# Performance work log

Hardware: AMD Instinct MI355X
Metric: run time of the kernel (lower is better)

The kernel has to match this reference:

```python
import jax, jax.numpy as jnp
import numpy as np

B, C_IN, C_OUT, E, K = 4, 32, 64, 200000, 5


def setup_inputs() -> dict:
    key = jax.random.key(0)
    k1, k2, k3, k4 = jax.random.split(key, 4)
    x = jax.random.normal(k1, (B, C_IN, E), dtype=jnp.float32)
    # Gi: per-edge [self_id, n1, n2, n3, n4] one-ring indices into the edge axis
    Gi = jax.random.randint(k2, (B, E, K), 0, E, dtype=jnp.int32)
    # Conv2d(C_IN, C_OUT, kernel_size=(1, K)) weights, PyTorch layout (O, I, 1, K)
    fan_in = C_IN * K
    bound = 1.0 / np.sqrt(fan_in)
    W = jax.random.uniform(k3, (C_OUT, C_IN, 1, K), jnp.float32, -bound, bound)
    b = jax.random.uniform(k4, (C_OUT,), jnp.float32, -bound, bound)
    return {"x": x, "Gi": Gi, "W": W, "b": b}


def _mesh_conv(x, Gi, W, b):
    Bn, C, En = x.shape
    # prepend zero-padding column (index 0 after Gi+1 maps to zeros)
    xp = jnp.concatenate([jnp.zeros((Bn, C, 1), x.dtype), x], axis=2)  # (B, C, E+1)
    idx = Gi.astype(jnp.int32) + 1  # (B, E, 5)
    # gather 1-ring neighbor features: f[b, c, e, j] = xp[b, c, idx[b, e, j]]
    f = jax.vmap(lambda xb, ib: xb[:, ib])(xp, idx)  # (B, C, E, 5)
    f0, f1, f2, f3, f4 = (f[..., j] for j in range(5))
    # symmetric, order-invariant combine
    G = jnp.stack([f0, f1 + f3, f2 + f4, jnp.abs(f1 - f3), jnp.abs(f2 - f4)], axis=3)
    # Conv2d with kernel (1, K), no padding -> contraction over (C_in, K)
    out = jnp.einsum('bcek,ock->boe', G, W[:, :, 0, :]) + b[None, :, None]
    return out[..., None]  # (B, C_out, E, 1)


def reference(x, Gi, W, b):
    return _mesh_conv(x, Gi, W, b)
```

## Files before the change

### kernel.cpp

```cpp
#include <hip/hip_runtime.h>

typedef unsigned int u32;
typedef __bf16 bf16x8 __attribute__((ext_vector_type(8)));
typedef float f32x4 __attribute__((ext_vector_type(4)));
typedef u32 u32x4 __attribute__((ext_vector_type(4)));

#define B_DIM 4
#define E_DIM 200000
#define C_OUT 64
#define TPB   12500
#define NTILE (B_DIM * TPB)
#define KPADW 168
#define ROWU  (KPADW / 2)
#define WLDS  (C_OUT * ROWU)

__device__ __forceinline__ u32 pack_bf2(float lo, float hi) {
  u32 a = __float_as_uint(lo) + 0x8000u;
  u32 b = __float_as_uint(hi) + 0x8000u;
  return __builtin_amdgcn_perm(b, a, 0x07060302u);
}

__device__ __forceinline__ u32 absdiff_pack(u32 a, u32 b) {
  float alo = __uint_as_float(a << 16), ahi = __uint_as_float(a & 0xffff0000u);
  float blo = __uint_as_float(b << 16), bhi = __uint_as_float(b & 0xffff0000u);
  u32 dlo = __float_as_uint(alo - blo) + 0x8000u;
  u32 dhi = __float_as_uint(ahi - bhi) + 0x8000u;
  return __builtin_amdgcn_perm(dhi, dlo, 0x07060302u) & 0x7fff7fffu;
}

__global__ __launch_bounds__(256) void xpose_kernel(const float* __restrict__ x,
                                                    u32* __restrict__ xT) {
  const int e = blockIdx.x * 256 + threadIdx.x;
  const int b = blockIdx.y;
  if (e >= E_DIM) return;
  const float* xb = x + (size_t)b * 32 * E_DIM;
  u32 row[16];
#pragma unroll
  for (int u = 0; u < 16; ++u) {
    const float lo = xb[(2 * u) * E_DIM + e];
    const float hi = xb[(2 * u + 1) * E_DIM + e];
    row[u] = pack_bf2(lo, hi);
  }
  uint4* dst = (uint4*)(xT + ((size_t)b * E_DIM + e) * 16);
#pragma unroll
  for (int w = 0; w < 4; ++w)
    dst[w] = make_uint4(row[4 * w], row[4 * w + 1], row[4 * w + 2], row[4 * w + 3]);
}

__global__ __launch_bounds__(256) void prep_w(const float* __restrict__ W,
                                              u32* __restrict__ Wa) {
  const int p = blockIdx.x * 256 + threadIdx.x;
  if (p >= C_OUT * 5 * 16) return;
  const int o = p / 80, r = p % 80, s = r / 16, cc = r % 16;
  const float w0 = W[(o * 32 + 2 * cc) * 5 + s];
  const float w1 = W[(o * 32 + 2 * cc + 1) * 5 + s];
  Wa[o * ROWU + s * 16 + cc] = pack_bf2(w0, w1);
}

__global__ __launch_bounds__(256, 4) void mesh_main(const u32* __restrict__ xT,
                                                    const int* __restrict__ Gi,
                                                    const u32* __restrict__ Wa,
                                                    const float* __restrict__ bias,
                                                    float* __restrict__ out) {
  __shared__ u32 Wl[WLDS];
  for (int i = threadIdx.x; i < WLDS; i += 256) Wl[i] = Wa[i];
  __syncthreads();

  const int l  = threadIdx.x & 63;
  const int wv = threadIdx.x >> 6;
  const int n  = l & 15;
  const int q  = l >> 4;
  const int j4 = l & 3;
  const int eL = l >> 2;
  const int pidx = ((n << 2) | q) << 2;
  const int NW = gridDim.x * 4;

  int t = blockIdx.x * 4 + wv;

  int b  = t / TPB;
  int e0 = (t - b * TPB) * 16;
  {
  }
  const int* gp = Gi + ((b * E_DIM + e0 + eL) * 5);
  int i0 = gp[0], i1 = gp[1], i2 = gp[2], i3 = gp[3], i4 = gp[4];
  const uint4* xb = (const uint4*)(xT + (size_t)b * E_DIM * 16);
  uint4 c0 = xb[i0 * 4 + j4], c1 = xb[i1 * 4 + j4], c2 = xb[i2 * 4 + j4],
        c3 = xb[i3 * 4 + j4], c4 = xb[i4 * 4 + j4];

  const f32x4* bp = (const f32x4*)bias;

  for (;;) {
    const int nt = t + NW;
    const bool has = nt < NTILE;
    int nb = 0, ne0 = 0;
    uint4 x0, x1, x2, x3, x4;
    if (has) {
      nb  = nt / TPB;
      ne0 = (nt - nb * TPB) * 16;
      const int* gq = Gi + ((nb * E_DIM + ne0 + eL) * 5);
      const int k0 = gq[0], k1 = gq[1], k2 = gq[2], k3 = gq[3], k4 = gq[4];
      const uint4* xn = (const uint4*)(xT + (size_t)nb * E_DIM * 16);
      x0 = xn[k0 * 4 + j4]; x1 = xn[k1 * 4 + j4]; x2 = xn[k2 * 4 + j4];
      x3 = xn[k3 * 4 + j4]; x4 = xn[k4 * 4 + j4];
    }

    u32 rows[7][4];
    rows[0][0] = c0.x; rows[0][1] = c0.y; rows[0][2] = c0.z; rows[0][3] = c0.w;
    rows[1][0] = c1.x; rows[1][1] = c1.y; rows[1][2] = c1.z; rows[1][3] = c1.w;
    rows[2][0] = c2.x; rows[2][1] = c2.y; rows[2][2] = c2.z; rows[2][3] = c2.w;
    rows[3][0] = c3.x; rows[3][1] = c3.y; rows[3][2] = c3.z; rows[3][3] = c3.w;
    rows[4][0] = c4.x; rows[4][1] = c4.y; rows[4][2] = c4.z; rows[4][3] = c4.w;
#pragma unroll
    for (int wd = 0; wd < 4; ++wd) {
      rows[5][wd] = absdiff_pack(rows[1][wd], rows[3][wd]);
      rows[6][wd] = absdiff_pack(rows[2][wd], rows[4][wd]);
    }

    f32x4 acc0 = bp[0 * 4 + q];
    f32x4 acc1 = bp[1 * 4 + q];
    f32x4 acc2 = bp[2 * 4 + q];
    f32x4 acc3 = bp[3 * 4 + q];

    const int aslot[7] = {0, 1, 2, 1, 2, 3, 4};
#pragma unroll
    for (int kc = 0; kc < 7; ++kc) {
      union { u32 u[4]; bf16x8 v; } bu;
#pragma unroll
      for (int c = 0; c < 4; ++c)
        bu.u[c] = (u32)__builtin_amdgcn_ds_bpermute(pidx, (int)rows[kc][c]);
      const int wbase = n * ROWU + aslot[kc] * 16 + q * 4;
      union { u32x4 u; bf16x8 v; } a0, a1, a2, a3;
      a0.u = *(const u32x4*)(Wl + wbase);
      a1.u = *(const u32x4*)(Wl + wbase + 16 * ROWU);
      a2.u = *(const u32x4*)(Wl + wbase + 32 * ROWU);
      a3.u = *(const u32x4*)(Wl + wbase + 48 * ROWU);
      acc0 = __builtin_amdgcn_mfma_f32_16x16x32_bf16(a0.v, bu.v, acc0, 0, 0, 0);
      acc1 = __builtin_amdgcn_mfma_f32_16x16x32_bf16(a1.v, bu.v, acc1, 0, 0, 0);
      acc2 = __builtin_amdgcn_mfma_f32_16x16x32_bf16(a2.v, bu.v, acc2, 0, 0, 0);
      acc3 = __builtin_amdgcn_mfma_f32_16x16x32_bf16(a3.v, bu.v, acc3, 0, 0, 0);
    }

    float* ob = out + ((b * C_OUT + q * 4) * E_DIM + e0 + n);
#pragma unroll
    for (int r = 0; r < 4; ++r) {
      ob[(0 * 16 + r) * E_DIM] = acc0[r];
      ob[(1 * 16 + r) * E_DIM] = acc1[r];
      ob[(2 * 16 + r) * E_DIM] = acc2[r];
      ob[(3 * 16 + r) * E_DIM] = acc3[r];
    }

    if (!has) break;
    t = nt; b = nb; e0 = ne0;
    c0 = x0; c1 = x1; c2 = x2; c3 = x3; c4 = x4;
  }
}

extern "C" void kernel_launch(void* const* d_in, const int* in_sizes, int n_in,
                              void* d_out, int out_size, void* d_ws, size_t ws_size,
                              hipStream_t stream) {
  const float* x    = (const float*)d_in[0];
  const int*   Gi   = (const int*)d_in[1];
  const float* W    = (const float*)d_in[2];
  const float* bias = (const float*)d_in[3];
  float* out = (float*)d_out;

  u32* xT = (u32*)d_ws;
  u32* Wa = xT + (size_t)B_DIM * E_DIM * 16;

  dim3 gx((E_DIM + 255) / 256, B_DIM);
  xpose_kernel<<<gx, 256, 0, stream>>>(x, xT);

  prep_w<<<(C_OUT * 5 * 16 + 255) / 256, 256, 0, stream>>>(W, Wa);

  mesh_main<<<1024, 256, 0, stream>>>(xT, Gi, Wa, bias, out);
}
```

Before: 459.0 us.

## Gather MFMA B-fragments directly, pre-swizzle weights, stage transpose through LDS

Each lane now loads the neighbor feature chunk it needs for the MFMA B operand straight from global memory, which removes the ds_bpermute shuffles. The weights are pre-expanded into 7 k-slices laid out per lane so LDS reads are contiguous uint4s. The transpose kernel now goes through LDS so its global stores are coalesced. The index prefetch runs two tiles ahead, the bias is hoisted into registers, and the grid size and occupancy bound change. The cost is more gather requests per lane pattern, higher register pressure, and a larger LDS weight buffer.

```diff
diff --git a/kernel.cpp b/kernel.cpp
--- a/kernel.cpp
+++ b/kernel.cpp
@@ -3,16 +3,14 @@
 typedef unsigned int u32;
 typedef __bf16 bf16x8 __attribute__((ext_vector_type(8)));
 typedef float f32x4 __attribute__((ext_vector_type(4)));
-typedef u32 u32x4 __attribute__((ext_vector_type(4)));
 
 #define B_DIM 4
 #define E_DIM 200000
 #define C_OUT 64
 #define TPB   12500
-#define NTILE (B_DIM * TPB)
-#define KPADW 168
-#define ROWU  (KPADW / 2)
-#define WLDS  (C_OUT * ROWU)
+#define NT    (B_DIM * TPB)
+#define NBLK  1280
+#define WLDS_U4 1792
 
 __device__ __forceinline__ u32 pack_bf2(float lo, float hi) {
   u32 a = __float_as_uint(lo) + 0x8000u;
@@ -28,130 +26,155 @@
   return __builtin_amdgcn_perm(dhi, dlo, 0x07060302u) & 0x7fff7fffu;
 }
 
+__device__ __forceinline__ uint4 absdiff_vec(uint4 a, uint4 b) {
+  return make_uint4(absdiff_pack(a.x, b.x), absdiff_pack(a.y, b.y),
+                    absdiff_pack(a.z, b.z), absdiff_pack(a.w, b.w));
+}
+
 __global__ __launch_bounds__(256) void xpose_kernel(const float* __restrict__ x,
                                                     u32* __restrict__ xT) {
-  const int e = blockIdx.x * 256 + threadIdx.x;
+  __shared__ u32 T[256 * 17];
   const int b = blockIdx.y;
-  if (e >= E_DIM) return;
-  const float* xb = x + (size_t)b * 32 * E_DIM;
-  u32 row[16];
+  const int e0 = blockIdx.x * 256;
+  const int t = threadIdx.x;
+  const int nrows = min(256, E_DIM - e0);
+  const float* xb = x + (size_t)b * 32 * E_DIM + e0;
+  if (t < nrows) {
 #pragma unroll
-  for (int u = 0; u < 16; ++u) {
-    const float lo = xb[(2 * u) * E_DIM + e];
-    const float hi = xb[(2 * u + 1) * E_DIM + e];
-    row[u] = pack_bf2(lo, hi);
+    for (int u = 0; u < 16; ++u) {
+      const float lo = xb[(size_t)(2 * u) * E_DIM + t];
+      const float hi = xb[(size_t)(2 * u + 1) * E_DIM + t];
+      T[t * 17 + u] = pack_bf2(lo, hi);
+    }
   }
-  uint4* dst = (uint4*)(xT + ((size_t)b * E_DIM + e) * 16);
+  __syncthreads();
+  const int total = nrows * 16;
+  u32* dst = xT + ((size_t)b * E_DIM + e0) * 16;
 #pragma unroll
-  for (int w = 0; w < 4; ++w)
-    dst[w] = make_uint4(row[4 * w], row[4 * w + 1], row[4 * w + 2], row[4 * w + 3]);
+  for (int k = 0; k < 16; ++k) {
+    const int g = t + k * 256;
+    if (g < total) dst[g] = T[(g >> 4) * 17 + (g & 15)];
+  }
 }
 
 __global__ __launch_bounds__(256) void prep_w(const float* __restrict__ W,
-                                              u32* __restrict__ Wa) {
+                                              u32* __restrict__ Wa2) {
   const int p = blockIdx.x * 256 + threadIdx.x;
-  if (p >= C_OUT * 5 * 16) return;
-  const int o = p / 80, r = p % 80, s = r / 16, cc = r % 16;
-  const float w0 = W[(o * 32 + 2 * cc) * 5 + s];
-  const float w1 = W[(o * 32 + 2 * cc + 1) * 5 + s];
-  Wa[o * ROWU + s * 16 + cc] = pack_bf2(w0, w1);
+  if (p >= 7168) return;
+  const int r = p & 3;
+  const int o = (p >> 2) & 63;
+  const int q = (p >> 8) & 3;
+  const int s = p >> 10;
+  const int kmap[7] = {0, 1, 2, 1, 2, 3, 4};
+  const int c0 = q * 8 + 2 * r;
+  const float w0 = W[(o * 32 + c0) * 5 + kmap[s]];
+  const float w1 = W[(o * 32 + c0 + 1) * 5 + kmap[s]];
+  Wa2[p] = pack_bf2(w0, w1);
 }
 
-__global__ __launch_bounds__(256, 4) void mesh_main(const u32* __restrict__ xT,
-                                                    const int* __restrict__ Gi,
-                                                    const u32* __restrict__ Wa,
-                                                    const float* __restrict__ bias,
-                                                    float* __restrict__ out) {
-  __shared__ u32 Wl[WLDS];
-  for (int i = threadIdx.x; i < WLDS; i += 256) Wl[i] = Wa[i];
+__global__ __launch_bounds__(256) void mesh_main(const u32* __restrict__ xT,
+                                                 const int* __restrict__ Gi,
+                                                 const u32* __restrict__ Wa2,
+                                                 const float* __restrict__ bias,
+                                                 float* __restrict__ out) {
+  __shared__ uint4 Wl[WLDS_U4];
+  {
+    const uint4* src = (const uint4*)Wa2;
+#pragma unroll
+    for (int k = 0; k < 7; ++k) Wl[threadIdx.x + k * 256] = src[threadIdx.x + k * 256];
+  }
   __syncthreads();
 
-  const int l  = threadIdx.x & 63;
+  const int l = threadIdx.x & 63;
   const int wv = threadIdx.x >> 6;
-  const int n  = l & 15;
-  const int q  = l >> 4;
-  const int j4 = l & 3;
-  const int eL = l >> 2;
-  const int pidx = ((n << 2) | q) << 2;
-  const int NW = gridDim.x * 4;
+  const int n = l & 15;
+  const int q = l >> 4;
+  const int NW = NBLK * 4;
+
+  f32x4 bv[4];
+#pragma unroll
+  for (int og = 0; og < 4; ++og) bv[og] = *(const f32x4*)(bias + og * 16 + q * 4);
+
+  const uint4* xb4 = (const uint4*)xT;
 
   int t = blockIdx.x * 4 + wv;
 
-  int b  = t / TPB;
-  int e0 = (t - b * TPB) * 16;
+  int gcur[5], gnext[5];
   {
+    const int b = t / TPB;
+    const int e = (t - b * TPB) * 16 + n;
+    const int* gp = Gi + (b * E_DIM + e) * 5;
+#pragma unroll
+    for (int s = 0; s < 5; ++s) gcur[s] = b * E_DIM + gp[s];
   }
-  const int* gp = Gi + ((b * E_DIM + e0 + eL) * 5);
-  int i0 = gp[0], i1 = gp[1], i2 = gp[2], i3 = gp[3], i4 = gp[4];
-  const uint4* xb = (const uint4*)(xT + (size_t)b * E_DIM * 16);
-  uint4 c0 = xb[i0 * 4 + j4], c1 = xb[i1 * 4 + j4], c2 = xb[i2 * 4 + j4],
-        c3 = xb[i3 * 4 + j4], c4 = xb[i4 * 4 + j4];
+  uint4 cur[5];
+#pragma unroll
+  for (int s = 0; s < 5; ++s) cur[s] = xb4[(size_t)gcur[s] * 4 + q];
 
-  const f32x4* bp = (const f32x4*)bias;
+  int t1 = t + NW;
+  if (t1 < NT) {
+    const int b = t1 / TPB;
+    const int e = (t1 - b * TPB) * 16 + n;
+    const int* gp = Gi + (b * E_DIM + e) * 5;
+#pragma unroll
+    for (int s = 0; s < 5; ++s) gnext[s] = b * E_DIM + gp[s];
+  }
 
   for (;;) {
-    const int nt = t + NW;
-    const bool has = nt < NTILE;
-    int nb = 0, ne0 = 0;
-    uint4 x0, x1, x2, x3, x4;
+    const bool has = t1 < NT;
+    uint4 nxt[5];
     if (has) {
-      nb  = nt / TPB;
-      ne0 = (nt - nb * TPB) * 16;
-      const int* gq = Gi + ((nb * E_DIM + ne0 + eL) * 5);
-      const int k0 = gq[0], k1 = gq[1], k2 = gq[2], k3 = gq[3], k4 = gq[4];
-      const uint4* xn = (const uint4*)(xT + (size_t)nb * E_DIM * 16);
-      x0 = xn[k0 * 4 + j4]; x1 = xn[k1 * 4 + j4]; x2 = xn[k2 * 4 + j4];
-      x3 = xn[k3 * 4 + j4]; x4 = xn[k4 * 4 + j4];
+#pragma unroll
+      for (int s = 0; s < 5; ++s) nxt[s] = xb4[(size_t)gnext[s] * 4 + q];
+    }
+    const int t2 = t1 + NW;
+    if (t2 < NT) {
+      const int b = t2 / TPB;
+      const int e = (t2 - b * TPB) * 16 + n;
+      const int* gp = Gi + (b * E_DIM + e) * 5;
+#pragma unroll
+      for (int s = 0; s < 5; ++s) gnext[s] = b * E_DIM + gp[s];
     }
 
-    u32 rows[7][4];
-    rows[0][0] = c0.x; rows[0][1] = c0.y; rows[0][2] = c0.z; rows[0][3] = c0.w;
-    rows[1][0] = c1.x; rows[1][1] = c1.y; rows[1][2] = c1.z; rows[1][3] = c1.w;
-    rows[2][0] = c2.x; rows[2][1] = c2.y; rows[2][2] = c2.z; rows[2][3] = c2.w;
-    rows[3][0] = c3.x; rows[3][1] = c3.y; rows[3][2] = c3.z; rows[3][3] = c3.w;
-    rows[4][0] = c4.x; rows[4][1] = c4.y; rows[4][2] = c4.z; rows[4][3] = c4.w;
+    union { uint4 u; bf16x8 v; } frag[7];
 #pragma unroll
-    for (int wd = 0; wd < 4; ++wd) {
-      rows[5][wd] = absdiff_pack(rows[1][wd], rows[3][wd]);
-      rows[6][wd] = absdiff_pack(rows[2][wd], rows[4][wd]);
+    for (int s = 0; s < 5; ++s) frag[s].u = cur[s];
+    frag[5].u = absdiff_vec(cur[1], cur[3]);
+    frag[6].u = absdiff_vec(cur[2], cur[4]);
+
+    f32x4 acc0 = bv[0], acc1 = bv[1], acc2 = bv[2], acc3 = bv[3];
+#pragma unroll
+    for (int c = 0; c < 7; ++c) {
+      const uint4* wp = Wl + (c * 4 + q) * 64 + n;
+      union { uint4 u; bf16x8 v; } a0, a1, a2, a3;
+      a0.u = wp[0];
+      a1.u = wp[16];
+      a2.u = wp[32];
+      a3.u = wp[48];
+      acc0 = __builtin_amdgcn_mfma_f32_16x16x32_bf16(a0.v, frag[c].v, acc0, 0, 0, 0);
+      acc1 = __builtin_amdgcn_mfma_f32_16x16x32_bf16(a1.v, frag[c].v, acc1, 0, 0, 0);
+      acc2 = __builtin_amdgcn_mfma_f32_16x16x32_bf16(a2.v, frag[c].v, acc2, 0, 0, 0);
+      acc3 = __builtin_amdgcn_mfma_f32_16x16x32_bf16(a3.v, frag[c].v, acc3, 0, 0, 0);
     }
 
-    f32x4 acc0 = bp[0 * 4 + q];
-    f32x4 acc1 = bp[1 * 4 + q];
-    f32x4 acc2 = bp[2 * 4 + q];
-    f32x4 acc3 = bp[3 * 4 + q];
-
-    const int aslot[7] = {0, 1, 2, 1, 2, 3, 4};
+    {
+      const int b = t / TPB;
+      const int e0 = (t - b * TPB) * 16;
+      float* ob = out + ((size_t)(b * C_OUT + q * 4) * E_DIM + e0 + n);
 #pragma unroll
-    for (int kc = 0; kc < 7; ++kc) {
-      union { u32 u[4]; bf16x8 v; } bu;
-#pragma unroll
-      for (int c = 0; c < 4; ++c)
-        bu.u[c] = (u32)__builtin_amdgcn_ds_bpermute(pidx, (int)rows[kc][c]);
-      const int wbase = n * ROWU + aslot[kc] * 16 + q * 4;
-      union { u32x4 u; bf16x8 v; } a0, a1, a2, a3;
-      a0.u = *(const u32x4*)(Wl + wbase);
-      a1.u = *(const u32x4*)(Wl + wbase + 16 * ROWU);
-      a2.u = *(const u32x4*)(Wl + wbase + 32 * ROWU);
-      a3.u = *(const u32x4*)(Wl + wbase + 48 * ROWU);
-      acc0 = __builtin_amdgcn_mfma_f32_16x16x32_bf16(a0.v, bu.v, acc0, 0, 0, 0);
-      acc1 = __builtin_amdgcn_mfma_f32_16x16x32_bf16(a1.v, bu.v, acc1, 0, 0, 0);
-      acc2 = __builtin_amdgcn_mfma_f32_16x16x32_bf16(a2.v, bu.v, acc2, 0, 0, 0);
-      acc3 = __builtin_amdgcn_mfma_f32_16x16x32_bf16(a3.v, bu.v, acc3, 0, 0, 0);
-    }
-
-    float* ob = out + ((b * C_OUT + q * 4) * E_DIM + e0 + n);
-#pragma unroll
-    for (int r = 0; r < 4; ++r) {
-      ob[(0 * 16 + r) * E_DIM] = acc0[r];
-      ob[(1 * 16 + r) * E_DIM] = acc1[r];
-      ob[(2 * 16 + r) * E_DIM] = acc2[r];
-      ob[(3 * 16 + r) * E_DIM] = acc3[r];
+      for (int r = 0; r < 4; ++r) {
+        ob[(size_t)(0 * 16 + r) * E_DIM] = acc0[r];
+        ob[(size_t)(1 * 16 + r) * E_DIM] = acc1[r];
+        ob[(size_t)(2 * 16 + r) * E_DIM] = acc2[r];
+        ob[(size_t)(3 * 16 + r) * E_DIM] = acc3[r];
+      }
     }
 
     if (!has) break;
-    t = nt; b = nb; e0 = ne0;
-    c0 = x0; c1 = x1; c2 = x2; c3 = x3; c4 = x4;
+    t = t1;
+    t1 = t2;
+#pragma unroll
+    for (int s = 0; s < 5; ++s) cur[s] = nxt[s];
   }
 }
 
@@ -164,13 +187,13 @@
   const float* bias = (const float*)d_in[3];
   float* out = (float*)d_out;
 
-  u32* xT = (u32*)d_ws;
-  u32* Wa = xT + (size_t)B_DIM * E_DIM * 16;
+  u32* xT  = (u32*)d_ws;
+  u32* Wa2 = xT + (size_t)B_DIM * E_DIM * 16;
 
   dim3 gx((E_DIM + 255) / 256, B_DIM);
   xpose_kernel<<<gx, 256, 0, stream>>>(x, xT);
 
-  prep_w<<<(C_OUT * 5 * 16 + 255) / 256, 256, 0, stream>>>(W, Wa);
+  prep_w<<<28, 256, 0, stream>>>(W, Wa2);
 
-  mesh_main<<<1024, 256, 0, stream>>>(xT, Gi, Wa, bias, out);
+  mesh_main<<<NBLK, 256, 0, stream>>>(xT, Gi, Wa2, bias, out);
 }
```

After: 392.9 us. -14.4%, faster.
